# Performance work log

Hardware: AMD Instinct MI355X
Metric: run time of the kernel (lower is better)

## Reference

```python
import jax, jax.numpy as jnp
import numpy as np

AXIS = 1          # reduction axis in the original input
KEEPDIM = False
INPUT_SHAPE = (4096, 2048)
B = 8             # leading grad-batch dim


def setup_inputs() -> dict:
    key = jax.random.key(0)
    k1, k2 = jax.random.split(key)
    grad_last = jax.random.normal(k1, (B, INPUT_SHAPE[0]), dtype=jnp.float32)
    indices = jax.random.randint(k2, (INPUT_SHAPE[0],), 0, INPUT_SHAPE[AXIS], dtype=jnp.int64)
    return {"grad_last": grad_last, "indices": indices}


def reference(grad_last, indices):
    # indices stored with a prepended grad-batch dim: [1, N]
    ind = indices[None, :]
    if not KEEPDIM:
        # unsqueeze at axis+1 (account for leading grad-batch dim)
        grad_last = jnp.expand_dims(grad_last, AXIS + 1)   # [B, N, 1]
        ind = jnp.expand_dims(ind, AXIS + 1)               # [1, N, 1]
    new_dim = INPUT_SHAPE[AXIS]
    # coord: iota along the reduced dim, broadcast against indices
    coord_shape = [1] * grad_last.ndim
    coord_shape[AXIS + 1] = new_dim
    coord = jnp.arange(new_dim).reshape(coord_shape)       # [1, 1, new_dim]
    mask = (coord == ind).astype(grad_last.dtype)          # [1, N, new_dim] -> broadcasts
    # one-hot scatter of grad to the argmax position: [B, N, new_dim]
    return mask * grad_last
```

## Files before the change

### kernel.cpp

```cpp
#include <hip/hip_runtime.h>


#define ROWS_PER_B 4096
#define NEWDIM     2048
#define F4_PER_ROW (NEWDIM / 4)
#define RPI        8
#define ITERS      4

typedef float f32x4 __attribute__((ext_vector_type(4)));

__global__ __launch_bounds__(512)
void ReduceMaxGrad_53833120088407_kernel(const float* __restrict__ grad,
                                         const int*  __restrict__ indices,
                                         float*      __restrict__ out) {
    const int t    = threadIdx.x;
    const int row0 = blockIdx.x * (RPI * ITERS);

    int   idx[RPI];
    float g[RPI];
#pragma unroll
    for (int r = 0; r < RPI; ++r) {
        idx[r] = indices[(row0 + r) & (ROWS_PER_B - 1)];
        g[r]   = grad[row0 + r];
    }

    f32x4* o = (f32x4*)out + (size_t)row0 * F4_PER_ROW + t;

#pragma unroll
    for (int it = 0; it < ITERS; ++it) {
        int   nidx[RPI];
        float ng[RPI];
        if (it + 1 < ITERS) {
            const int nrow0 = row0 + (it + 1) * RPI;
#pragma unroll
            for (int r = 0; r < RPI; ++r) {
                nidx[r] = indices[(nrow0 + r) & (ROWS_PER_B - 1)];
                ng[r]   = grad[nrow0 + r];
            }
        }
#pragma unroll
        for (int r = 0; r < RPI; ++r) {
            f32x4 v = (f32x4)(0.f);
            if ((idx[r] >> 2) == t) v[idx[r] & 3] = g[r];
            o[(size_t)(it * RPI + r) * F4_PER_ROW] = v;
        }
        if (it + 1 < ITERS) {
#pragma unroll
            for (int r = 0; r < RPI; ++r) { idx[r] = nidx[r]; g[r] = ng[r]; }
        }
    }
}

extern "C" void kernel_launch(void* const* d_in, const int* in_sizes, int n_in,
                              void* d_out, int out_size, void* d_ws, size_t ws_size,
                              hipStream_t stream) {
    const float* grad    = (const float*)d_in[0];
    const int*   indices = (const int*)d_in[1];
    float*       out     = (float*)d_out;

    const int n_rows   = in_sizes[0];
    const int n_blocks = n_rows / (RPI * ITERS);
    ReduceMaxGrad_53833120088407_kernel<<<dim3(n_blocks), dim3(512), 0, stream>>>(
        grad, indices, out);
}
```

Measured before the change: 254.8 us.

## Remap work to grid-strided rows with 256-thread blocks and branchless stores

```diff
diff --git a/kernel.cpp b/kernel.cpp
--- a/kernel.cpp
+++ b/kernel.cpp
@@ -4,50 +4,42 @@
 #define ROWS_PER_B 4096
 #define NEWDIM     2048
 #define F4_PER_ROW (NEWDIM / 4)
-#define RPI        8
-#define ITERS      4
+#define NTHREADS   524288
+#define ITERS      32
 
 typedef float f32x4 __attribute__((ext_vector_type(4)));
 
-__global__ __launch_bounds__(512)
+__global__ __launch_bounds__(256)
 void ReduceMaxGrad_53833120088407_kernel(const float* __restrict__ grad,
                                          const int*  __restrict__ indices,
                                          float*      __restrict__ out) {
-    const int t    = threadIdx.x;
-    const int row0 = blockIdx.x * (RPI * ITERS);
+    const int gtid     = blockIdx.x * 256 + threadIdx.x;
+    const int c4       = gtid & (F4_PER_ROW - 1);
+    const int row_base = gtid >> 9;
+    const int c4x4     = c4 << 2;
 
-    int   idx[RPI];
-    float g[RPI];
-#pragma unroll
-    for (int r = 0; r < RPI; ++r) {
-        idx[r] = indices[(row0 + r) & (ROWS_PER_B - 1)];
-        g[r]   = grad[row0 + r];
-    }
+    f32x4* o = (f32x4*)out + gtid;
 
-    f32x4* o = (f32x4*)out + (size_t)row0 * F4_PER_ROW + t;
+    int   idx = indices[row_base & (ROWS_PER_B - 1)];
+    float g   = grad[row_base];
 
 #pragma unroll
-    for (int it = 0; it < ITERS; ++it) {
-        int   nidx[RPI];
-        float ng[RPI];
-        if (it + 1 < ITERS) {
-            const int nrow0 = row0 + (it + 1) * RPI;
-#pragma unroll
-            for (int r = 0; r < RPI; ++r) {
-                nidx[r] = indices[(nrow0 + r) & (ROWS_PER_B - 1)];
-                ng[r]   = grad[nrow0 + r];
-            }
+    for (int i = 0; i < ITERS; ++i) {
+        int   nidx = 0;
+        float ng   = 0.0f;
+        if (i + 1 < ITERS) {
+            const int nrow = (i + 1) * 1024 + row_base;
+            nidx = indices[nrow & (ROWS_PER_B - 1)];
+            ng   = grad[nrow];
         }
-#pragma unroll
-        for (int r = 0; r < RPI; ++r) {
-            f32x4 v = (f32x4)(0.f);
-            if ((idx[r] >> 2) == t) v[idx[r] & 3] = g[r];
-            o[(size_t)(it * RPI + r) * F4_PER_ROW] = v;
-        }
-        if (it + 1 < ITERS) {
-#pragma unroll
-            for (int r = 0; r < RPI; ++r) { idx[r] = nidx[r]; g[r] = ng[r]; }
-        }
+        const int c = idx - c4x4;
+        f32x4 v;
+        v.x = (c == 0) ? g : 0.0f;
+        v.y = (c == 1) ? g : 0.0f;
+        v.z = (c == 2) ? g : 0.0f;
+        v.w = (c == 3) ? g : 0.0f;
+        o[(size_t)i * NTHREADS] = v;
+        idx = nidx; g = ng;
     }
 }
 
@@ -58,8 +50,6 @@
     const int*   indices = (const int*)d_in[1];
     float*       out     = (float*)d_out;
 
-    const int n_rows   = in_sizes[0];
-    const int n_blocks = n_rows / (RPI * ITERS);
-    ReduceMaxGrad_53833120088407_kernel<<<dim3(n_blocks), dim3(512), 0, stream>>>(
+    ReduceMaxGrad_53833120088407_kernel<<<dim3(2048), dim3(256), 0, stream>>>(
         grad, indices, out);
 }
```

Result: no change. 257.2 us (+1.0%).
